# Kernel tuning notes

Hardware: AMD Instinct MI355X
Metric: run time of the kernel (lower is better)

## Reference

```python
import jax, jax.numpy as jnp
import numpy as np

N_MLP = 16
LATENT = 1024
S0, S1, S2, OUT = 512, 256, 128, 3


def _make_grid(n_grid_step):
    # matches np.meshgrid (indexing='xy') then reshape(-1): points (x, y)
    p = np.linspace(-1.0, 1.0, n_grid_step, dtype=np.float32)
    X, Y = np.meshgrid(p, p)
    return jnp.asarray(np.stack([X.ravel(), Y.ravel()], axis=-1))  # [G, 2]


def setup_inputs() -> dict:
    key = jax.random.key(0)
    ks = jax.random.split(key, 12)
    sc = lambda fan_in: 1.0 / np.sqrt(fan_in)
    inp = {
        "x0": jax.random.normal(ks[0], (LATENT,), jnp.float32),
        "W0a": jax.random.normal(ks[1], (N_MLP, S0, LATENT), jnp.float32) * sc(LATENT),
        "b0a": jax.random.normal(ks[2], (N_MLP, S0), jnp.float32) * sc(LATENT),
        "W0b": jax.random.normal(ks[3], (N_MLP, S0, 2), jnp.float32) * sc(2),
        "b0b": jax.random.normal(ks[4], (N_MLP, S0), jnp.float32) * sc(2),
        "W1": jax.random.normal(ks[5], (N_MLP, S1, S0), jnp.float32) * sc(S0),
        "b1": jax.random.normal(ks[6], (N_MLP, S1), jnp.float32) * sc(S0),
        "W2": jax.random.normal(ks[7], (N_MLP, S2, S1), jnp.float32) * sc(S1),
        "b2": jax.random.normal(ks[8], (N_MLP, S2), jnp.float32) * sc(S1),
        "W3": jax.random.normal(ks[9], (N_MLP, OUT, S2), jnp.float32) * sc(S2),
        "b3": jax.random.normal(ks[10], (N_MLP, OUT), jnp.float32) * sc(S2),
        "n_grid_step": 128,
    }
    return inp


def reference(x0, W0a, b0a, W0b, b0b, W1, b1, W2, b2, W3, b3, n_grid_step):
    grid = _make_grid(n_grid_step)  # [G, 2], constant (requires_grad=False)
    # latent branch: [m, S0]
    y0_a = jnp.einsum('mol,l->mo', W0a, x0) + b0a
    # grid branch: [m, G, S0]
    y0_b = jnp.einsum('moi,gi->mgo', W0b, grid) + b0b[:, None, :]
    h = jax.nn.relu(y0_a[:, None, :] + y0_b)                        # [m,G,S0]
    h = jax.nn.relu(jnp.einsum('moh,mgh->mgo', W1, h) + b1[:, None, :])  # [m,G,S1]
    h = jax.nn.relu(jnp.einsum('moh,mgh->mgo', W2, h) + b2[:, None, :])  # [m,G,S2]
    out = jnp.tanh(jnp.einsum('moh,mgh->mgo', W3, h) + b3[:, None, :])   # [m,G,3]
    return out.reshape(-1, OUT)  # [m*G, 3]
```

## Files before the change

kernel.cpp:

```cpp
#include <hip/hip_runtime.h>
#include <hip/hip_bf16.h>
#include <cstdint>

typedef __bf16 bf16_t;
typedef bf16_t bf16x8 __attribute__((ext_vector_type(8)));
typedef bf16_t bf16x4 __attribute__((ext_vector_type(4)));
typedef float  f32x4  __attribute__((ext_vector_type(4)));

#define S0 512
#define S1 256
#define S2 128
#define NGRID 128
#define GPTS (NGRID*NGRID)

#define WS_BASE 0u
#define WS_W1P  32768u
#define WS_W2P  (32768u + 4194304u)
#define WS_W3P  (32768u + 4194304u + 1048576u)

__device__ __forceinline__ float tanh_fast(float x) {
  float e = __builtin_amdgcn_exp2f(x * 2.88539008f);
  return fmaf(-2.0f, __builtin_amdgcn_rcpf(e + 1.0f), 1.0f);
}

__global__ __launch_bounds__(256) void prep_k(
    const float* __restrict__ x0, const float* __restrict__ W0a,
    const float* __restrict__ b0a, const float* __restrict__ b0b,
    const float* __restrict__ W1, const float* __restrict__ W2,
    const float* __restrict__ W3, float* __restrict__ base,
    bf16_t* __restrict__ W1p, bf16_t* __restrict__ W2p, bf16_t* __restrict__ W3p)
{
  if (blockIdx.x < 2048) {
    int wid = (blockIdx.x << 2) + (threadIdx.x >> 6);
    int L = threadIdx.x & 63;
    int m = wid >> 9, o = wid & 511;
    const float* wrow = W0a + ((size_t)(m*S0 + o) << 10);
    float acc = 0.f;
#pragma unroll
    for (int i = 0; i < 4; ++i) {
      f32x4 wv = *(const f32x4*)(wrow + i*256 + L*4);
      f32x4 xv = *(const f32x4*)(x0   + i*256 + L*4);
      acc += wv.x*xv.x + wv.y*xv.y + wv.z*xv.z + wv.w*xv.w;
    }
#pragma unroll
    for (int s = 32; s; s >>= 1) acc += __shfl_xor(acc, s, 64);
    if (L == 0) base[m*S0 + o] = acc + b0a[m*S0 + o] + b0b[m*S0 + o];
    return;
  }

  int T = (blockIdx.x - 2048) * 256 + threadIdx.x;
  const float* src = nullptr;
  bf16_t* dst = nullptr;
  if (T < 262144) {
    int L = T & 63, nt = (T >> 6) & 15, ks = (T >> 10) & 15, m = T >> 14;
    int n = nt*16 + (L & 15), k0 = ks*32 + ((L >> 4) & 3)*8;
    src = W1 + (size_t)(m*S1 + n)*S0 + k0;
    dst = W1p + (size_t)T*8;
  } else if (T < 262144 + 65536) {
    int T2 = T - 262144;
    int L = T2 & 63, nt = (T2 >> 6) & 7, ks = (T2 >> 9) & 7, m = T2 >> 12;
    int n = nt*16 + (L & 15), k0 = ks*32 + ((L >> 4) & 3)*8;
    src = W2 + (size_t)(m*S2 + n)*S1 + k0;
    dst = W2p + (size_t)T2*8;
  } else {
    int T3 = T - 327680;
    int L = T3 & 63, ks = (T3 >> 6) & 3, m = T3 >> 8;
    int n = L & 15, k0 = ks*32 + ((L >> 4) & 3)*8;
    dst = W3p + (size_t)T3*8;
    if (n < 3) src = W3 + (size_t)(m*3 + n)*S2 + k0;
  }
  bf16x8 v;
  if (src) {
    f32x4 a = *(const f32x4*)src;
    f32x4 b = *(const f32x4*)(src + 4);
    v[0]=(bf16_t)a.x; v[1]=(bf16_t)a.y; v[2]=(bf16_t)a.z; v[3]=(bf16_t)a.w;
    v[4]=(bf16_t)b.x; v[5]=(bf16_t)b.y; v[6]=(bf16_t)b.z; v[7]=(bf16_t)b.w;
  } else {
#pragma unroll
    for (int j = 0; j < 8; ++j) v[j] = (bf16_t)0.f;
  }
  *(bf16x8*)dst = v;
}

__global__ __launch_bounds__(256, 3) void fused_mlp_k(
    const float* __restrict__ base, const float* __restrict__ W0b,
    const bf16_t* __restrict__ W1p, const bf16_t* __restrict__ W2p,
    const bf16_t* __restrict__ W3p,
    const float* __restrict__ b1, const float* __restrict__ b2,
    const float* __restrict__ b3, float* __restrict__ out)
{
  __shared__ __align__(16) bf16_t sA1[64*264];

  const int bid  = blockIdx.x;
  const int m    = bid >> 8;
  const int tile = bid & 255;
  const int g0   = tile * 64;

  const int tid  = threadIdx.x;
  const int w    = tid >> 6, L = tid & 63;
  const int quad = L >> 4, lrow = L & 15;

  const float step = 2.0f / 127.0f;
  const float yv  = -1.0f + (float)(tile >> 1) * step;
  const float xv0 = -1.0f + (float)(((tile & 1) << 6) + lrow) * step;

  const float* basep = base + m*S0;
  const float* w0bp  = W0b + (size_t)m*S0*2;

  f32x4 zero = {0.f, 0.f, 0.f, 0.f};
  f32x4 acc1[4][4];
#pragma unroll
  for (int a = 0; a < 4; ++a)
#pragma unroll
    for (int b = 0; b < 4; ++b) acc1[a][b] = zero;

  const bf16_t* bp1 = W1p + (((size_t)(m*16)*16 + w*4)*64 + L)*8;
  bf16x8 Bc[4];
#pragma unroll
  for (int n = 0; n < 4; ++n) Bc[n] = *(const bf16x8*)(bp1 + (size_t)n*512);

#pragma unroll 2
  for (int ks = 0; ks < 16; ++ks) {
    const int kk = ks*32 + quad*8;
    f32x4 cA  = *(const f32x4*)(basep + kk);
    f32x4 cB  = *(const f32x4*)(basep + kk + 4);
    f32x4 wv0 = *(const f32x4*)(w0bp + kk*2);
    f32x4 wv1 = *(const f32x4*)(w0bp + kk*2 + 4);
    f32x4 wv2 = *(const f32x4*)(w0bp + kk*2 + 8);
    f32x4 wv3 = *(const f32x4*)(w0bp + kk*2 + 12);

    bf16x8 Bn[4];
    if (ks < 15) {
#pragma unroll
      for (int n = 0; n < 4; ++n)
        Bn[n] = *(const bf16x8*)(bp1 + (size_t)(ks+1)*8192 + (size_t)n*512);
    }

    float t[8], wx[8];
    t[0] = fmaf(wv0.y, yv, cA.x); wx[0] = wv0.x;
    t[1] = fmaf(wv0.w, yv, cA.y); wx[1] = wv0.z;
    t[2] = fmaf(wv1.y, yv, cA.z); wx[2] = wv1.x;
    t[3] = fmaf(wv1.w, yv, cA.w); wx[3] = wv1.z;
    t[4] = fmaf(wv2.y, yv, cB.x); wx[4] = wv2.x;
    t[5] = fmaf(wv2.w, yv, cB.y); wx[5] = wv2.z;
    t[6] = fmaf(wv3.y, yv, cB.z); wx[6] = wv3.x;
    t[7] = fmaf(wv3.w, yv, cB.w); wx[7] = wv3.z;

#pragma unroll
    for (int mt = 0; mt < 4; ++mt) {
      const float xr = xv0 + (float)(mt*16)*step;
      bf16x8 af;
#pragma unroll
      for (int j = 0; j < 8; ++j)
        af[j] = (bf16_t)fmaxf(fmaf(wx[j], xr, t[j]), 0.f);
#pragma unroll
      for (int n = 0; n < 4; ++n)
        acc1[mt][n] = __builtin_amdgcn_mfma_f32_16x16x32_bf16(Bc[n], af, acc1[mt][n], 0, 0, 0);
    }
    if (ks < 15) {
#pragma unroll
      for (int n = 0; n < 4; ++n) Bc[n] = Bn[n];
    }
  }

#pragma unroll
  for (int nb = 0; nb < 4; ++nb) {
    const int col = w*64 + nb*16 + quad*4;
    f32x4 bb = *(const f32x4*)(b1 + m*S1 + col);
#pragma unroll
    for (int mt = 0; mt < 4; ++mt) {
      const int row = mt*16 + lrow;
      bf16x4 v;
#pragma unroll
      for (int p = 0; p < 4; ++p)
        v[p] = (bf16_t)fmaxf(acc1[mt][nb][p] + bb[p], 0.f);
      *(bf16x4*)(&sA1[row*264 + col]) = v;
    }
  }
  __syncthreads();

  f32x4 acc2[4][2];
#pragma unroll
  for (int a = 0; a < 4; ++a) { acc2[a][0] = zero; acc2[a][1] = zero; }
  const bf16_t* bp2 = W2p + (((size_t)(m*8)*8 + w*2)*64 + L)*8;
#pragma unroll 2
  for (int ks = 0; ks < 8; ++ks) {
    const int k2 = ks*32 + quad*8;
    bf16x8 af[4];
#pragma unroll
    for (int mt = 0; mt < 4; ++mt)
      af[mt] = *(const bf16x8*)(&sA1[(mt*16 + lrow)*264 + k2]);
    bf16x8 b0f = *(const bf16x8*)(bp2 + (size_t)ks*4096);
    bf16x8 b1f = *(const bf16x8*)(bp2 + (size_t)ks*4096 + 512);
#pragma unroll
    for (int mt = 0; mt < 4; ++mt)
      acc2[mt][0] = __builtin_amdgcn_mfma_f32_16x16x32_bf16(b0f, af[mt], acc2[mt][0], 0, 0, 0);
#pragma unroll
    for (int mt = 0; mt < 4; ++mt)
      acc2[mt][1] = __builtin_amdgcn_mfma_f32_16x16x32_bf16(b1f, af[mt], acc2[mt][1], 0, 0, 0);
  }
  __syncthreads();

  bf16_t* sH2 = sA1;
#pragma unroll
  for (int nb = 0; nb < 2; ++nb) {
    const int col = w*32 + nb*16 + quad*4;
    f32x4 bb = *(const f32x4*)(b2 + m*S2 + col);
#pragma unroll
    for (int mt = 0; mt < 4; ++mt) {
      const int row = mt*16 + lrow;
      bf16x4 v;
#pragma unroll
      for (int p = 0; p < 4; ++p)
        v[p] = (bf16_t)fmaxf(acc2[mt][nb][p] + bb[p], 0.f);
      *(bf16x4*)(&sH2[row*136 + col]) = v;
    }
  }
  __syncthreads();

  f32x4 acc3 = zero;
#pragma unroll
  for (int ks = 0; ks < 4; ++ks) {
    bf16x8 af  = *(const bf16x8*)(&sH2[(w*16 + lrow)*136 + ks*32 + quad*8]);
    bf16x8 bfr = *(const bf16x8*)(W3p + (((size_t)m*4 + ks)*64 + L)*8);
    acc3 = __builtin_amdgcn_mfma_f32_16x16x32_bf16(bfr, af, acc3, 0, 0, 0);
  }
  if (quad == 0) {
    const size_t o = ((size_t)m*GPTS + g0 + w*16 + lrow)*3;
    out[o + 0] = tanh_fast(acc3[0] + b3[m*3 + 0]);
    out[o + 1] = tanh_fast(acc3[1] + b3[m*3 + 1]);
    out[o + 2] = tanh_fast(acc3[2] + b3[m*3 + 2]);
  }
}

extern "C" void kernel_launch(void* const* d_in, const int* in_sizes, int n_in,
                              void* d_out, int out_size, void* d_ws, size_t ws_size,
                              hipStream_t stream) {
  const float* x0  = (const float*)d_in[0];
  const float* W0a = (const float*)d_in[1];
  const float* b0a = (const float*)d_in[2];
  const float* W0b = (const float*)d_in[3];
  const float* b0b = (const float*)d_in[4];
  const float* W1  = (const float*)d_in[5];
  const float* b1  = (const float*)d_in[6];
  const float* W2  = (const float*)d_in[7];
  const float* b2  = (const float*)d_in[8];
  const float* W3  = (const float*)d_in[9];
  const float* b3  = (const float*)d_in[10];

  char* ws = (char*)d_ws;
  float*  base = (float*)(ws + WS_BASE);
  bf16_t* W1p  = (bf16_t*)(ws + WS_W1P);
  bf16_t* W2p  = (bf16_t*)(ws + WS_W2P);
  bf16_t* W3p  = (bf16_t*)(ws + WS_W3P);
  float*  out  = (float*)d_out;

  prep_k<<<3344, 256, 0, stream>>>(x0, W0a, b0a, b0b, W1, W2, W3, base, W1p, W2p, W3p);
  fused_mlp_k<<<4096, 256, 0, stream>>>(base, W0b, W1p, W2p, W3p, b1, b2, b3, out);
}
```

Baseline: 212.5 us.

## Classify layer-0 neurons by grid bounds; skip dead, fold always-active, compact the rest

A new classification kernel uses interval bounds over the [-1,1]^2 grid to sort first-layer neurons into always-dead, always-active and ambiguous. Dead neurons are dropped. Always-active neurons are folded through W1 into a per-output affine term in x and y, built with atomics in a new prep kernel. Only ambiguous neurons are compacted and packed into the bf16 W1 tiles, so the dominant layer-1 MFMA loop runs a data-dependent, shorter K. This trades two extra small launches and gather loads for fewer layer-1 MFMAs, and also raises the occupancy hint to 4.

```diff
diff --git a/kernel.cpp b/kernel.cpp
--- a/kernel.cpp
+++ b/kernel.cpp
@@ -13,22 +13,27 @@
 #define NGRID 128
 #define GPTS (NGRID*NGRID)
 
-#define WS_BASE 0u
-#define WS_W1P  32768u
-#define WS_W2P  (32768u + 4194304u)
-#define WS_W3P  (32768u + 4194304u + 1048576u)
+#define WS_BASE  0u
+#define WS_W1P   32768u
+#define WS_W2P   4227072u
+#define WS_W3P   5275648u
+#define WS_BASEC 5341184u
+#define WS_WXYC  5373952u
+#define WS_IDX   5439488u
+#define WS_LIN   5472256u
+#define WS_F     5505024u
+#define WS_CNT   5570560u
 
 __device__ __forceinline__ float tanh_fast(float x) {
   float e = __builtin_amdgcn_exp2f(x * 2.88539008f);
   return fmaf(-2.0f, __builtin_amdgcn_rcpf(e + 1.0f), 1.0f);
 }
 
-__global__ __launch_bounds__(256) void prep_k(
+__global__ __launch_bounds__(256) void prep_a(
     const float* __restrict__ x0, const float* __restrict__ W0a,
     const float* __restrict__ b0a, const float* __restrict__ b0b,
-    const float* __restrict__ W1, const float* __restrict__ W2,
-    const float* __restrict__ W3, float* __restrict__ base,
-    bf16_t* __restrict__ W1p, bf16_t* __restrict__ W2p, bf16_t* __restrict__ W3p)
+    const float* __restrict__ W2, const float* __restrict__ W3,
+    float* __restrict__ base, bf16_t* __restrict__ W2p, bf16_t* __restrict__ W3p)
 {
   if (blockIdx.x < 2048) {
     int wid = (blockIdx.x << 2) + (threadIdx.x >> 6);
@@ -51,19 +56,13 @@
   int T = (blockIdx.x - 2048) * 256 + threadIdx.x;
   const float* src = nullptr;
   bf16_t* dst = nullptr;
-  if (T < 262144) {
-    int L = T & 63, nt = (T >> 6) & 15, ks = (T >> 10) & 15, m = T >> 14;
-    int n = nt*16 + (L & 15), k0 = ks*32 + ((L >> 4) & 3)*8;
-    src = W1 + (size_t)(m*S1 + n)*S0 + k0;
-    dst = W1p + (size_t)T*8;
-  } else if (T < 262144 + 65536) {
-    int T2 = T - 262144;
-    int L = T2 & 63, nt = (T2 >> 6) & 7, ks = (T2 >> 9) & 7, m = T2 >> 12;
+  if (T < 65536) {
+    int L = T & 63, nt = (T >> 6) & 7, ks = (T >> 9) & 7, m = T >> 12;
     int n = nt*16 + (L & 15), k0 = ks*32 + ((L >> 4) & 3)*8;
     src = W2 + (size_t)(m*S2 + n)*S1 + k0;
-    dst = W2p + (size_t)T2*8;
+    dst = W2p + (size_t)T*8;
   } else {
-    int T3 = T - 327680;
+    int T3 = T - 65536;
     int L = T3 & 63, ks = (T3 >> 6) & 3, m = T3 >> 8;
     int n = L & 15, k0 = ks*32 + ((L >> 4) & 3)*8;
     dst = W3p + (size_t)T3*8;
@@ -82,8 +81,108 @@
   *(bf16x8*)dst = v;
 }
 
-__global__ __launch_bounds__(256, 3) void fused_mlp_k(
+__global__ __launch_bounds__(256) void classify_k(
     const float* __restrict__ base, const float* __restrict__ W0b,
+    float* __restrict__ basec, float* __restrict__ wxyc,
+    int* __restrict__ idx, int* __restrict__ lin,
+    int* __restrict__ Kc, int* __restrict__ nlin, float* __restrict__ F)
+{
+  __shared__ int sc[512];
+  const int m = blockIdx.x, t = threadIdx.x;
+  float b[2], wx[2], wy[2]; int fa[2], fl[2];
+#pragma unroll
+  for (int h = 0; h < 2; ++h) {
+    const int k = t + h*256;
+    b[h]  = base[m*S0 + k];
+    wx[h] = W0b[(m*S0 + k)*2];
+    wy[h] = W0b[(m*S0 + k)*2 + 1];
+    const float aw = fabsf(wx[h]) + fabsf(wy[h]);
+    const int dead = (b[h] + aw) <= 0.f;
+    fl[h] = (!dead) && ((b[h] - aw) >= 0.f);
+    fa[h] = (!dead) && (!fl[h]);
+    sc[k] = fa[h] | (fl[h] << 16);
+  }
+  __syncthreads();
+  for (int off = 1; off < 512; off <<= 1) {
+    int v0 = sc[t], v1 = sc[t+256];
+    int u0 = (t >= off) ? sc[t-off] : 0;
+    int u1 = (t+256 >= off) ? sc[t+256-off] : 0;
+    __syncthreads();
+    sc[t] = v0 + u0; sc[t+256] = v1 + u1;
+    __syncthreads();
+  }
+  const int tot = sc[511];
+  const int KcM = tot & 0xffff, nlM = tot >> 16;
+#pragma unroll
+  for (int h = 0; h < 2; ++h) {
+    const int k = t + h*256;
+    const int incl = sc[k];
+    if (fa[h]) {
+      const int p = (incl & 0xffff) - 1;
+      idx[m*S0 + p] = k;
+      basec[m*S0 + p] = b[h];
+      wxyc[m*S0*2 + 2*p]     = wx[h];
+      wxyc[m*S0*2 + 2*p + 1] = wy[h];
+    } else if (fl[h]) {
+      lin[m*S0 + ((incl >> 16) - 1)] = k;
+    }
+  }
+  for (int s = t; s < 512; s += 256) {
+    if (s >= KcM) {
+      idx[m*S0 + s] = 0;
+      basec[m*S0 + s] = 0.f;
+      wxyc[m*S0*2 + 2*s] = 0.f;
+      wxyc[m*S0*2 + 2*s + 1] = 0.f;
+    }
+  }
+  for (int i = t; i < 1024; i += 256) F[m*1024 + i] = 0.f;
+  if (t == 0) { Kc[m] = KcM; nlin[m] = nlM; }
+}
+
+__global__ __launch_bounds__(256) void prep_b(
+    const float* __restrict__ W1, const float* __restrict__ base,
+    const float* __restrict__ W0b,
+    const int* __restrict__ idx, const int* __restrict__ lin,
+    const int* __restrict__ Kc, const int* __restrict__ nlin,
+    bf16_t* __restrict__ W1p, float* __restrict__ F)
+{
+  if (blockIdx.x < 1024) {
+    const int T = blockIdx.x*256 + threadIdx.x;
+    const int L = T & 63, nt = (T >> 6) & 15, ks = (T >> 10) & 15, m = T >> 14;
+    const int KcM = Kc[m];
+    const int nks = (KcM + 31) >> 5;
+    if (ks >= nks) return;
+    const int n = nt*16 + (L & 15), kb = ks*32 + ((L >> 4) & 3)*8;
+    const float* wrow = W1 + (size_t)(m*S1 + n)*S0;
+    const int* ip = idx + m*S0 + kb;
+    bf16x8 v;
+#pragma unroll
+    for (int j = 0; j < 8; ++j)
+      v[j] = (kb + j < KcM) ? (bf16_t)wrow[ip[j]] : (bf16_t)0.f;
+    *(bf16x8*)(W1p + (size_t)T*8) = v;
+  } else {
+    const int b2 = blockIdx.x - 1024;
+    const int m = b2 >> 4, s = b2 & 15, n = threadIdx.x;
+    const int nl = nlin[m];
+    float a0 = 0.f, ax = 0.f, ay = 0.f;
+    const float* wrow = W1 + (size_t)(m*S1 + n)*S0;
+    for (int j = s; j < nl; j += 16) {
+      const int k = lin[m*S0 + j];
+      const float w = wrow[k];
+      a0 = fmaf(w, base[m*S0 + k], a0);
+      ax = fmaf(w, W0b[(m*S0 + k)*2], ax);
+      ay = fmaf(w, W0b[(m*S0 + k)*2 + 1], ay);
+    }
+    float* fp = F + ((size_t)m*S1 + n)*4;
+    atomicAdd(fp + 0, a0);
+    atomicAdd(fp + 1, ax);
+    atomicAdd(fp + 2, ay);
+  }
+}
+
+__global__ __launch_bounds__(256, 4) void fused_mlp_k(
+    const float* __restrict__ basec, const float* __restrict__ wxyc,
+    const float* __restrict__ F, const int* __restrict__ Kc,
     const bf16_t* __restrict__ W1p, const bf16_t* __restrict__ W2p,
     const bf16_t* __restrict__ W3p,
     const float* __restrict__ b1, const float* __restrict__ b2,
@@ -104,8 +203,9 @@
   const float yv  = -1.0f + (float)(tile >> 1) * step;
   const float xv0 = -1.0f + (float)(((tile & 1) << 6) + lrow) * step;
 
-  const float* basep = base + m*S0;
-  const float* w0bp  = W0b + (size_t)m*S0*2;
+  const float* bc = basec + m*S0;
+  const float* wc = wxyc + m*(S0*2);
+  const int nks = (Kc[m] + 31) >> 5;
 
   f32x4 zero = {0.f, 0.f, 0.f, 0.f};
   f32x4 acc1[4][4];
@@ -120,17 +220,17 @@
   for (int n = 0; n < 4; ++n) Bc[n] = *(const bf16x8*)(bp1 + (size_t)n*512);
 
 #pragma unroll 2
-  for (int ks = 0; ks < 16; ++ks) {
+  for (int ks = 0; ks < nks; ++ks) {
     const int kk = ks*32 + quad*8;
-    f32x4 cA  = *(const f32x4*)(basep + kk);
-    f32x4 cB  = *(const f32x4*)(basep + kk + 4);
-    f32x4 wv0 = *(const f32x4*)(w0bp + kk*2);
-    f32x4 wv1 = *(const f32x4*)(w0bp + kk*2 + 4);
-    f32x4 wv2 = *(const f32x4*)(w0bp + kk*2 + 8);
-    f32x4 wv3 = *(const f32x4*)(w0bp + kk*2 + 12);
+    f32x4 cA  = *(const f32x4*)(bc + kk);
+    f32x4 cB  = *(const f32x4*)(bc + kk + 4);
+    f32x4 wv0 = *(const f32x4*)(wc + kk*2);
+    f32x4 wv1 = *(const f32x4*)(wc + kk*2 + 4);
+    f32x4 wv2 = *(const f32x4*)(wc + kk*2 + 8);
+    f32x4 wv3 = *(const f32x4*)(wc + kk*2 + 12);
 
     bf16x8 Bn[4];
-    if (ks < 15) {
+    if (ks + 1 < nks) {
 #pragma unroll
       for (int n = 0; n < 4; ++n)
         Bn[n] = *(const bf16x8*)(bp1 + (size_t)(ks+1)*8192 + (size_t)n*512);
@@ -157,7 +257,7 @@
       for (int n = 0; n < 4; ++n)
         acc1[mt][n] = __builtin_amdgcn_mfma_f32_16x16x32_bf16(Bc[n], af, acc1[mt][n], 0, 0, 0);
     }
-    if (ks < 15) {
+    if (ks + 1 < nks) {
 #pragma unroll
       for (int n = 0; n < 4; ++n) Bc[n] = Bn[n];
     }
@@ -167,13 +267,21 @@
   for (int nb = 0; nb < 4; ++nb) {
     const int col = w*64 + nb*16 + quad*4;
     f32x4 bb = *(const f32x4*)(b1 + m*S1 + col);
+    float cterm[4], fx[4];
+#pragma unroll
+    for (int p = 0; p < 4; ++p) {
+      f32x4 Fv = *(const f32x4*)(F + ((size_t)m*S1 + col + p)*4);
+      cterm[p] = fmaf(Fv.z, yv, bb[p] + Fv.x);
+      fx[p] = Fv.y;
+    }
 #pragma unroll
     for (int mt = 0; mt < 4; ++mt) {
       const int row = mt*16 + lrow;
+      const float xr = xv0 + (float)(mt*16)*step;
       bf16x4 v;
 #pragma unroll
       for (int p = 0; p < 4; ++p)
-        v[p] = (bf16_t)fmaxf(acc1[mt][nb][p] + bb[p], 0.f);
+        v[p] = (bf16_t)fmaxf(acc1[mt][nb][p] + fmaf(fx[p], xr, cterm[p]), 0.f);
       *(bf16x4*)(&sA1[row*264 + col]) = v;
     }
   }
@@ -249,12 +357,21 @@
   const float* b3  = (const float*)d_in[10];
 
   char* ws = (char*)d_ws;
-  float*  base = (float*)(ws + WS_BASE);
-  bf16_t* W1p  = (bf16_t*)(ws + WS_W1P);
-  bf16_t* W2p  = (bf16_t*)(ws + WS_W2P);
-  bf16_t* W3p  = (bf16_t*)(ws + WS_W3P);
-  float*  out  = (float*)d_out;
-
-  prep_k<<<3344, 256, 0, stream>>>(x0, W0a, b0a, b0b, W1, W2, W3, base, W1p, W2p, W3p);
-  fused_mlp_k<<<4096, 256, 0, stream>>>(base, W0b, W1p, W2p, W3p, b1, b2, b3, out);
-}
+  float*  base  = (float*)(ws + WS_BASE);
+  bf16_t* W1p   = (bf16_t*)(ws + WS_W1P);
+  bf16_t* W2p   = (bf16_t*)(ws + WS_W2P);
+  bf16_t* W3p   = (bf16_t*)(ws + WS_W3P);
+  float*  basec = (float*)(ws + WS_BASEC);
+  float*  wxyc  = (float*)(ws + WS_WXYC);
+  int*    idx   = (int*)(ws + WS_IDX);
+  int*    lin   = (int*)(ws + WS_LIN);
+  float*  F     = (float*)(ws + WS_F);
+  int*    Kc    = (int*)(ws + WS_CNT);
+  int*    nlin  = (int*)(ws + WS_CNT + 64);
+  float*  out   = (float*)d_out;
+
+  prep_a<<<2368, 256, 0, stream>>>(x0, W0a, b0a, b0b, W2, W3, base, W2p, W3p);
+  classify_k<<<16, 256, 0, stream>>>(base, W0b, basec, wxyc, idx, lin, Kc, nlin, F);
+  prep_b<<<1280, 256, 0, stream>>>(W1, base, W0b, idx, lin, Kc, nlin, W1p, F);
+  fused_mlp_k<<<4096, 256, 0, stream>>>(basec, wxyc, F, Kc, W1p, W2p, W3p, b1, b2, b3, out);
+}
```

Result: slower. 258.4 us (+21.6%).
